# Performance work log

Measured on AMD Instinct MI355X. Metric: run time of the kernel, lower is better.

## Reference

```python
import jax, jax.numpy as jnp
import numpy as np

N = 50000      # nodes
E = 800000     # edges (before self-loops)
NFEAT = 128
NHID = 32
H = 8
NCLASS = 47
NEG_SLOPE = 0.2  # PyG GATv2Conv default


def gatv2_layer(x, src, dst, Wl, Wr, att, b, n):
    """One GATv2Conv layer (concat over heads). att: [H, C]."""
    h, c = att.shape
    xl = (x @ Wl).reshape(n, h, c)  # source transform (lin_l)
    xr = (x @ Wr).reshape(n, h, c)  # target transform (lin_r)
    e = jax.nn.leaky_relu(xl[src] + xr[dst], NEG_SLOPE)   # [E, H, C]
    logits = jnp.einsum('ehc,hc->eh', e, att)             # [E, H]
    # segment softmax over incoming edges of each target node
    m = jax.ops.segment_max(logits, dst, num_segments=n)  # [N, H]
    alpha = jnp.exp(logits - m[dst])
    denom = jax.ops.segment_sum(alpha, dst, num_segments=n)
    alpha = alpha / (denom[dst] + 1e-16)
    msg = xl[src] * alpha[:, :, None]                     # [E, H, C]
    out = jax.ops.segment_sum(msg, dst, num_segments=n)   # [N, H, C]
    return out.reshape(n, h * c) + b


def setup_inputs():
    key = jax.random.key(0)
    ks = jax.random.split(key, 16)
    s = 0.1
    x = jax.random.normal(ks[0], (N, NFEAT), jnp.float32)
    edge_index = jax.random.randint(ks[1], (2, E), 0, N)
    HID = H * NHID  # 256
    params = dict(
        Wl0=jax.random.normal(ks[2], (NFEAT, HID), jnp.float32) * s,
        Wr0=jax.random.normal(ks[3], (NFEAT, HID), jnp.float32) * s,
        a0=jax.random.normal(ks[4], (H, NHID), jnp.float32) * s,
        b0=jnp.zeros((HID,), jnp.float32),
        Wl1=jax.random.normal(ks[5], (HID, HID), jnp.float32) * s,
        Wr1=jax.random.normal(ks[6], (HID, HID), jnp.float32) * s,
        a1=jax.random.normal(ks[7], (H, NHID), jnp.float32) * s,
        b1=jnp.zeros((HID,), jnp.float32),
        Wl2=jax.random.normal(ks[8], (HID, NCLASS), jnp.float32) * s,
        Wr2=jax.random.normal(ks[9], (HID, NCLASS), jnp.float32) * s,
        a2=jax.random.normal(ks[10], (1, NCLASS), jnp.float32) * s,
        b2=jnp.zeros((NCLASS,), jnp.float32),
    )
    return {"x": x, "edge_index": edge_index, **params}


def reference(x, edge_index, Wl0, Wr0, a0, b0, Wl1, Wr1, a1, b1, Wl2, Wr2, a2, b2):
    n = x.shape[0]
    # PyG GATv2Conv adds self-loops by default
    loops = jnp.arange(n, dtype=edge_index.dtype)
    src = jnp.concatenate([edge_index[0], loops])
    dst = jnp.concatenate([edge_index[1], loops])
    h = gatv2_layer(x, src, dst, Wl0, Wr0, a0, b0, n)
    h = jax.nn.elu(h)
    h = gatv2_layer(h, src, dst, Wl1, Wr1, a1, b1, n)
    h = jax.nn.elu(h)
    h = gatv2_layer(h, src, dst, Wl2, Wr2, a2, b2, n)
    return jax.nn.log_softmax(h, axis=-1)
```

## Files before the change

kernel.cpp:

```cpp
#include <hip/hip_runtime.h>
#include <cmath>


#define NFEAT 128
#define HID 256
#define NCLS 47
#define L2PAD 64

typedef __attribute__((ext_vector_type(8))) short bf16x8;
typedef __attribute__((ext_vector_type(4))) float f32x4;
typedef __attribute__((ext_vector_type(2))) float f32x2;

__device__ __forceinline__ unsigned short f2b(float f) {
  unsigned int u = __builtin_bit_cast(unsigned int, f);
  u += 0x7FFFu + ((u >> 16) & 1u);
  return (unsigned short)(u >> 16);
}
__device__ __forceinline__ float b2f(unsigned short s) {
  return __builtin_bit_cast(float, (unsigned int)s << 16);
}
__device__ __forceinline__ f32x2 b2f2(unsigned int u) {
  return (f32x2){__builtin_bit_cast(float, u << 16),
                 __builtin_bit_cast(float, u & 0xFFFF0000u)};
}

__global__ void k_cast_bf16(const float* __restrict__ in,
                            unsigned short* __restrict__ out, int n4) {
  int i = blockIdx.x * blockDim.x + threadIdx.x;
  if (i < n4) {
    float4 v = reinterpret_cast<const float4*>(in)[i];
    ushort4 o = {f2b(v.x), f2b(v.y), f2b(v.z), f2b(v.w)};
    reinterpret_cast<ushort4*>(out)[i] = o;
  }
}

__global__ void k_wt(const float* __restrict__ W, unsigned short* __restrict__ WT,
                     int K, int M, int Mpad) {
  int i = blockIdx.x * blockDim.x + threadIdx.x;
  if (i >= Mpad * K) return;
  int m = i / K, k = i - m * K;
  WT[i] = (m < M) ? f2b(W[(size_t)k * M + m]) : 0;
}

__global__ void k_pad_att(const float* __restrict__ a, float* __restrict__ out48) {
  int i = threadIdx.x;
  if (i < 48) out48[i] = (i < NCLS) ? a[i] : 0.f;
}

__global__ void k_init_deg(int* __restrict__ deg, int n) {
  int i = blockIdx.x * blockDim.x + threadIdx.x;
  if (i < n) deg[i] = 1;
}

__global__ void k_count(const int* __restrict__ dst, int* __restrict__ deg, int e) {
  int i = blockIdx.x * blockDim.x + threadIdx.x;
  if (i < e) atomicAdd(&deg[dst[i]], 1);
}

__global__ __launch_bounds__(256) void k_bsum(const int* __restrict__ deg,
                                              int* __restrict__ bsum, int n) {
  int t = threadIdx.x;
  int base = blockIdx.x * 1024 + t * 4;
  int s = 0;
  if (base + 3 < n) {
    int4 v = *reinterpret_cast<const int4*>(deg + base);
    s = v.x + v.y + v.z + v.w;
  } else {
    for (int j = 0; j < 4; ++j) { int i = base + j; if (i < n) s += deg[i]; }
  }
  #pragma unroll
  for (int off = 1; off < 64; off <<= 1) s += __shfl_xor(s, off, 64);
  __shared__ int wsum[4];
  if ((t & 63) == 0) wsum[t >> 6] = s;
  __syncthreads();
  if (t == 0) bsum[blockIdx.x] = wsum[0] + wsum[1] + wsum[2] + wsum[3];
}

__global__ void k_scanb(int* __restrict__ bsum, int nb) {
  int lane = threadIdx.x;
  int v = (lane < nb) ? bsum[lane] : 0;
  #pragma unroll
  for (int off = 1; off < 64; off <<= 1) {
    int u = __shfl_up(v, off, 64);
    if (lane >= off) v += u;
  }
  if (lane < nb) bsum[lane] = v;
}

__global__ __launch_bounds__(256) void k_scanfinal(const int* __restrict__ deg,
                                                   const int* __restrict__ bscan,
                                                   int* __restrict__ rowptr, int n) {
  int t = threadIdx.x, b = blockIdx.x;
  int base = b * 1024 + t * 4;
  int v0 = 0, v1 = 0, v2 = 0, v3 = 0;
  if (base + 3 < n) {
    int4 v = *reinterpret_cast<const int4*>(deg + base);
    v0 = v.x; v1 = v.y; v2 = v.z; v3 = v.w;
  } else {
    if (base < n) v0 = deg[base];
    if (base + 1 < n) v1 = deg[base + 1];
    if (base + 2 < n) v2 = deg[base + 2];
    if (base + 3 < n) v3 = deg[base + 3];
  }
  int s = v0 + v1 + v2 + v3;
  int incl = s;
  #pragma unroll
  for (int off = 1; off < 64; off <<= 1) {
    int u = __shfl_up(incl, off, 64);
    if ((t & 63) >= off) incl += u;
  }
  __shared__ int wsum[4];
  int w = t >> 6, l = t & 63;
  if (l == 63) wsum[w] = incl;
  __syncthreads();
  int woff = 0;
  for (int j = 0; j < w; ++j) woff += wsum[j];
  int excl = incl - s + woff;
  int boff = (b == 0) ? 0 : bscan[b - 1];
  int p = boff + excl;
  if (base < n)     rowptr[base + 1] = p + v0;
  if (base + 1 < n) rowptr[base + 2] = p + v0 + v1;
  if (base + 2 < n) rowptr[base + 3] = p + v0 + v1 + v2;
  if (base + 3 < n) rowptr[base + 4] = p + v0 + v1 + v2 + v3;
  if (b == 0 && t == 0) rowptr[0] = 0;
}

__global__ void k_init_csr(const int* __restrict__ rowptr, int* __restrict__ adj,
                           int* __restrict__ vdst, int* __restrict__ cursor, int n) {
  int i = blockIdx.x * blockDim.x + threadIdx.x;
  if (i < n) { int p = rowptr[i]; adj[p] = i; vdst[p] = i; cursor[i] = p + 1; }
}

__global__ void k_scatter(const int* __restrict__ src, const int* __restrict__ dst,
                          int* __restrict__ cursor, int* __restrict__ adj,
                          int* __restrict__ vdst, int e) {
  int i = blockIdx.x * blockDim.x + threadIdx.x;
  if (i < e) {
    int d = dst[i];
    int p = atomicAdd(&cursor[d], 1);
    adj[p] = src[i];
    vdst[p] = d;
  }
}

__global__ __launch_bounds__(256) void gemm_dual_bf16(
    const unsigned short* __restrict__ X, const unsigned short* __restrict__ WlT,
    const unsigned short* __restrict__ WrT, unsigned short* __restrict__ XL,
    unsigned short* __restrict__ XR, int N, int K, int Mpad) {
  __shared__ __align__(16) unsigned short Xs[64][72];
  __shared__ __align__(16) unsigned short Ls[64][72];
  __shared__ __align__(16) unsigned short Rs[64][72];

  const int t = threadIdx.x;
  const int row0 = blockIdx.x * 64;
  const int col0 = blockIdx.y * 64;
  const int w = t >> 6, lane = t & 63;
  const int r15 = lane & 15, kc = lane >> 4;

  f32x4 accL[4], accR[4];
  #pragma unroll
  for (int i = 0; i < 4; ++i) {
    accL[i] = (f32x4){0.f, 0.f, 0.f, 0.f};
    accR[i] = (f32x4){0.f, 0.f, 0.f, 0.f};
  }

  for (int k0 = 0; k0 < K; k0 += 64) {
    #pragma unroll
    for (int cc = 0; cc < 2; ++cc) {
      int c = t + cc * 256;
      int row = c >> 3, seg = (c & 7) * 8;
      int grow = row0 + row;
      if (grow < N) {
        *reinterpret_cast<uint4*>(&Xs[row][seg]) =
            *reinterpret_cast<const uint4*>(X + (size_t)grow * K + k0 + seg);
      } else {
        *reinterpret_cast<uint4*>(&Xs[row][seg]) = (uint4){0, 0, 0, 0};
      }
      *reinterpret_cast<uint4*>(&Ls[row][seg]) =
          *reinterpret_cast<const uint4*>(WlT + (size_t)(col0 + row) * K + k0 + seg);
      *reinterpret_cast<uint4*>(&Rs[row][seg]) =
          *reinterpret_cast<const uint4*>(WrT + (size_t)(col0 + row) * K + k0 + seg);
    }
    __syncthreads();

    #pragma unroll
    for (int ks = 0; ks < 2; ++ks) {
      const bf16x8 a = *reinterpret_cast<const bf16x8*>(&Xs[16 * w + r15][ks * 32 + kc * 8]);
      #pragma unroll
      for (int nf = 0; nf < 4; ++nf) {
        const bf16x8 bl = *reinterpret_cast<const bf16x8*>(&Ls[nf * 16 + r15][ks * 32 + kc * 8]);
        const bf16x8 br = *reinterpret_cast<const bf16x8*>(&Rs[nf * 16 + r15][ks * 32 + kc * 8]);
        accL[nf] = __builtin_amdgcn_mfma_f32_16x16x32_bf16(a, bl, accL[nf], 0, 0, 0);
        accR[nf] = __builtin_amdgcn_mfma_f32_16x16x32_bf16(a, br, accR[nf], 0, 0, 0);
      }
    }
    __syncthreads();
  }

  #pragma unroll
  for (int nf = 0; nf < 4; ++nf) {
    int cc = col0 + nf * 16 + r15;
    #pragma unroll
    for (int i = 0; i < 4; ++i) {
      int rr = row0 + 16 * w + kc * 4 + i;
      if (rr < N) {
        XL[(size_t)rr * Mpad + cc] = f2b(accL[nf][i]);
        XR[(size_t)rr * Mpad + cc] = f2b(accR[nf][i]);
      }
    }
  }
}

__global__ __launch_bounds__(256) void gat_node_hc(
    const unsigned short* __restrict__ xl, const unsigned short* __restrict__ xr,
    const float* __restrict__ att, const float* __restrict__ bias,
    const int* __restrict__ rowptr, const int* __restrict__ adj,
    unsigned short* __restrict__ out, int n) {
  int wid = (blockIdx.x * blockDim.x + threadIdx.x) >> 6;
  int lane = threadIdx.x & 63;
  if (wid >= n) return;
  const int q = lane & 31, half = lane >> 5;

  const uint4 xrp = *reinterpret_cast<const uint4*>(xr + (size_t)wid * HID + q * 8);
  const f32x2 xr2[4] = {b2f2(xrp.x), b2f2(xrp.y), b2f2(xrp.z), b2f2(xrp.w)};
  const float4 af0 = *reinterpret_cast<const float4*>(att + q * 8);
  const float4 af1 = *reinterpret_cast<const float4*>(att + q * 8 + 4);
  const f32x2 a2[4] = {{af0.x, af0.y}, {af0.z, af0.w},
                       {af1.x, af1.y}, {af1.z, af1.w}};

  float m = -1e30f, denom = 0.f;
  f32x2 acc[4] = {{0.f, 0.f}, {0.f, 0.f}, {0.f, 0.f}, {0.f, 0.f}};

  const int beg = rowptr[wid], end = rowptr[wid + 1];
  for (int base = beg; base < end; base += 2) {
    const int i = base + half;
    const bool act = i < end;
    const int u = adj[act ? i : base];
    const uint4 p = *reinterpret_cast<const uint4*>(xl + (size_t)u * HID + q * 8);
    const f32x2 x2[4] = {b2f2(p.x), b2f2(p.y), b2f2(p.z), b2f2(p.w)};
    f32x2 s2 = x2[0] * 0.f;
    #pragma unroll
    for (int j = 0; j < 4; ++j) {
      f32x2 z = x2[j] + xr2[j];
      f32x2 lz = 0.2f * z;
      f32x2 r = {fmaxf(z.x, lz.x), fmaxf(z.y, lz.y)};
      s2 += r * a2[j];
    }
    float part = s2.x + s2.y;
    part += __shfl_xor(part, 1, 64);
    part += __shfl_xor(part, 2, 64);
    if (!act) part = -1e30f;
    if (__any(part > m + 8.f)) {
      float mn = fmaxf(m, part);
      float so = __expf(m - mn);
      float wn = act ? __expf(part - mn) : 0.f;
      denom = denom * so + wn;
      #pragma unroll
      for (int j = 0; j < 4; ++j) acc[j] = acc[j] * so + wn * x2[j];
      m = mn;
    } else {
      float wn = act ? __expf(part - m) : 0.f;
      denom += wn;
      #pragma unroll
      for (int j = 0; j < 4; ++j) acc[j] += wn * x2[j];
    }
  }

  float mo = __shfl_xor(m, 32, 64);
  float ms = fmaxf(m, mo);
  float sc = __expf(m - ms);
  denom *= sc;
  denom += __shfl_xor(denom, 32, 64);
  #pragma unroll
  for (int j = 0; j < 4; ++j) {
    acc[j] *= sc;
    acc[j].x += __shfl_xor(acc[j].x, 32, 64);
    acc[j].y += __shfl_xor(acc[j].y, 32, 64);
  }

  if (half == 0) {
    const float inv = 1.f / (denom + 1e-16f);
    const float4 bf0 = *reinterpret_cast<const float4*>(bias + q * 8);
    const float4 bf1 = *reinterpret_cast<const float4*>(bias + q * 8 + 4);
    float o[8] = {acc[0].x * inv + bf0.x, acc[0].y * inv + bf0.y,
                  acc[1].x * inv + bf0.z, acc[1].y * inv + bf0.w,
                  acc[2].x * inv + bf1.x, acc[2].y * inv + bf1.y,
                  acc[3].x * inv + bf1.z, acc[3].y * inv + bf1.w};
    #pragma unroll
    for (int j = 0; j < 8; ++j) o[j] = o[j] > 0.f ? o[j] : (__expf(o[j]) - 1.f);
    uint4 ov;
    ov.x = (unsigned)f2b(o[0]) | ((unsigned)f2b(o[1]) << 16);
    ov.y = (unsigned)f2b(o[2]) | ((unsigned)f2b(o[3]) << 16);
    ov.z = (unsigned)f2b(o[4]) | ((unsigned)f2b(o[5]) << 16);
    ov.w = (unsigned)f2b(o[6]) | ((unsigned)f2b(o[7]) << 16);
    *reinterpret_cast<uint4*>(out + (size_t)wid * HID + q * 8) = ov;
  }
}

__global__ __launch_bounds__(256) void k_logit_l2(
    const unsigned short* __restrict__ xl, const unsigned short* __restrict__ xr,
    const float* __restrict__ att48, const int* __restrict__ adj,
    const int* __restrict__ vdst, float* __restrict__ logit, int total) {
  int i = blockIdx.x * blockDim.x + threadIdx.x;
  if (i >= total) return;
  const int u = adj[i], v = vdst[i];
  const uint4* pu = reinterpret_cast<const uint4*>(xl + (size_t)u * L2PAD);
  const uint4* pv = reinterpret_cast<const uint4*>(xr + (size_t)v * L2PAD);
  f32x2 s2 = {0.f, 0.f};
  #pragma unroll
  for (int b = 0; b < 6; ++b) {
    const uint4 xu = pu[b], xv = pv[b];
    const f32x2* a2 = reinterpret_cast<const f32x2*>(att48 + b * 8);
    const unsigned ua[4] = {xu.x, xu.y, xu.z, xu.w};
    const unsigned va[4] = {xv.x, xv.y, xv.z, xv.w};
    #pragma unroll
    for (int j = 0; j < 4; ++j) {
      f32x2 z = b2f2(ua[j]) + b2f2(va[j]);
      f32x2 lz = 0.2f * z;
      f32x2 r = {fmaxf(z.x, lz.x), fmaxf(z.y, lz.y)};
      s2 += r * a2[j];
    }
  }
  logit[i] = s2.x + s2.y;
}

__global__ __launch_bounds__(256) void gat_node_l2(
    const unsigned short* __restrict__ xl, const float* __restrict__ logit,
    const float* __restrict__ bias, const int* __restrict__ rowptr,
    const int* __restrict__ adj, float* __restrict__ out, int n) {
  int wid = (blockIdx.x * blockDim.x + threadIdx.x) >> 6;
  int lane = threadIdx.x & 63;
  if (wid >= n) return;
  const bool act = lane < NCLS;
  const int beg = rowptr[wid], end = rowptr[wid + 1];

  float mx = -1e30f;
  for (int i = beg + lane; i < end; i += 64) mx = fmaxf(mx, logit[i]);
  #pragma unroll
  for (int off = 1; off < 64; off <<= 1) mx = fmaxf(mx, __shfl_xor(mx, off, 64));

  float denom = 0.f, acc = 0.f;
  int i = beg;
  for (; i + 1 < end; i += 2) {
    int u0 = adj[i], u1 = adj[i + 1];
    float w0 = __expf(logit[i] - mx);
    float w1 = __expf(logit[i + 1] - mx);
    float x0 = act ? b2f(xl[(size_t)u0 * L2PAD + lane]) : 0.f;
    float x1 = act ? b2f(xl[(size_t)u1 * L2PAD + lane]) : 0.f;
    denom += w0 + w1;
    acc += w0 * x0 + w1 * x1;
  }
  if (i < end) {
    int u0 = adj[i];
    float w0 = __expf(logit[i] - mx);
    float x0 = act ? b2f(xl[(size_t)u0 * L2PAD + lane]) : 0.f;
    denom += w0;
    acc += w0 * x0;
  }

  float r = acc / (denom + 1e-16f) + (act ? bias[lane] : 0.f);
  float rm = act ? r : -1e30f;
  #pragma unroll
  for (int off = 1; off < 64; off <<= 1) rm = fmaxf(rm, __shfl_xor(rm, off, 64));
  float se = act ? __expf(r - rm) : 0.f;
  #pragma unroll
  for (int off = 1; off < 64; off <<= 1) se += __shfl_xor(se, off, 64);
  if (act) out[(size_t)wid * NCLS + lane] = r - rm - __logf(se);
}

extern "C" void kernel_launch(void* const* d_in, const int* in_sizes, int n_in,
                              void* d_out, int out_size, void* d_ws, size_t ws_size,
                              hipStream_t stream) {
  const float* x   = (const float*)d_in[0];
  const int* ei    = (const int*)d_in[1];
  const float* Wl0 = (const float*)d_in[2];
  const float* Wr0 = (const float*)d_in[3];
  const float* a0  = (const float*)d_in[4];
  const float* b0  = (const float*)d_in[5];
  const float* Wl1 = (const float*)d_in[6];
  const float* Wr1 = (const float*)d_in[7];
  const float* a1  = (const float*)d_in[8];
  const float* b1  = (const float*)d_in[9];
  const float* Wl2 = (const float*)d_in[10];
  const float* Wr2 = (const float*)d_in[11];
  const float* a2  = (const float*)d_in[12];
  const float* b2  = (const float*)d_in[13];

  const int N = in_sizes[0] / NFEAT;
  const int E = in_sizes[1] / 2;
  const int* src = ei;
  const int* dst = ei + E;
  const int total = E + N;

  char* ws = (char*)d_ws;
  unsigned short* xlb = (unsigned short*)ws; ws += (size_t)N * HID * 2;
  unsigned short* xrb = (unsigned short*)ws; ws += (size_t)N * HID * 2;
  unsigned short* xb  = (unsigned short*)ws; ws += (size_t)N * HID * 2;
  unsigned short* hb  = (unsigned short*)ws; ws += (size_t)N * HID * 2;
  unsigned short* WT  = (unsigned short*)ws; ws += (size_t)6 * HID * HID * 2;
  float* logit = (float*)ws; ws += (size_t)total * sizeof(float);
  float* att48 = (float*)ws; ws += 64 * sizeof(float);
  int* deg    = (int*)ws; ws += (size_t)N * sizeof(int);
  int* rowptr = (int*)ws; ws += (size_t)(N + 8) * sizeof(int);
  int* bsum   = (int*)ws; ws += (size_t)64 * sizeof(int);
  int* adj    = (int*)ws; ws += (size_t)total * sizeof(int);
  int* vdst   = (int*)ws; ws += (size_t)total * sizeof(int);

  unsigned short* WlT0 = WT + 0 * HID * HID;
  unsigned short* WrT0 = WT + 1 * HID * HID;
  unsigned short* WlT1 = WT + 2 * HID * HID;
  unsigned short* WrT1 = WT + 3 * HID * HID;
  unsigned short* WlT2 = WT + 4 * HID * HID;
  unsigned short* WrT2 = WT + 5 * HID * HID;

  const int TB = 256;
  const int nbScan = (N + 1023) / 1024;

  k_cast_bf16<<<(N * NFEAT / 4 + TB - 1) / TB, TB, 0, stream>>>(x, xb, N * NFEAT / 4);
  k_wt<<<(HID * NFEAT + TB - 1) / TB, TB, 0, stream>>>(Wl0, WlT0, NFEAT, HID, HID);
  k_wt<<<(HID * NFEAT + TB - 1) / TB, TB, 0, stream>>>(Wr0, WrT0, NFEAT, HID, HID);
  k_wt<<<(HID * HID + TB - 1) / TB, TB, 0, stream>>>(Wl1, WlT1, HID, HID, HID);
  k_wt<<<(HID * HID + TB - 1) / TB, TB, 0, stream>>>(Wr1, WrT1, HID, HID, HID);
  k_wt<<<(L2PAD * HID + TB - 1) / TB, TB, 0, stream>>>(Wl2, WlT2, HID, NCLS, L2PAD);
  k_wt<<<(L2PAD * HID + TB - 1) / TB, TB, 0, stream>>>(Wr2, WrT2, HID, NCLS, L2PAD);
  k_pad_att<<<1, 64, 0, stream>>>(a2, att48);

  k_init_deg<<<(N + TB - 1) / TB, TB, 0, stream>>>(deg, N);
  k_count<<<(E + TB - 1) / TB, TB, 0, stream>>>(dst, deg, E);
  k_bsum<<<nbScan, TB, 0, stream>>>(deg, bsum, N);
  k_scanb<<<1, 64, 0, stream>>>(bsum, nbScan);
  k_scanfinal<<<nbScan, TB, 0, stream>>>(deg, bsum, rowptr, N);
  k_init_csr<<<(N + TB - 1) / TB, TB, 0, stream>>>(rowptr, adj, vdst, deg, N);
  k_scatter<<<(E + TB - 1) / TB, TB, 0, stream>>>(src, dst, deg, adj, vdst, E);

  const int nodeBlocks = (N + 3) / 4;
  const int rowBlocks = (N + 63) / 64;

  {
    dim3 g(rowBlocks, HID / 64);
    gemm_dual_bf16<<<g, 256, 0, stream>>>(xb, WlT0, WrT0, xlb, xrb, N, NFEAT, HID);
    gat_node_hc<<<nodeBlocks, 256, 0, stream>>>(xlb, xrb, a0, b0, rowptr, adj, hb, N);
  }
  {
    dim3 g(rowBlocks, HID / 64);
    gemm_dual_bf16<<<g, 256, 0, stream>>>(hb, WlT1, WrT1, xlb, xrb, N, HID, HID);
    gat_node_hc<<<nodeBlocks, 256, 0, stream>>>(xlb, xrb, a1, b1, rowptr, adj, xb, N);
  }
  {
    dim3 g(rowBlocks, 1);
    gemm_dual_bf16<<<g, 256, 0, stream>>>(xb, WlT2, WrT2, xlb, xrb, N, HID, L2PAD);
    k_logit_l2<<<(total + TB - 1) / TB, TB, 0, stream>>>(xlb, xrb, att48, adj,
                                                         vdst, logit, total);
    gat_node_l2<<<nodeBlocks, 256, 0, stream>>>(xlb, logit, b2, rowptr, adj,
                                                (float*)d_out, N);
  }
}
```

Measured before the change: 445.1 us.

## Use direct global-to-LDS loads with XOR swizzle, unroll edge loop, merge weight transposes

```diff
diff --git a/kernel.cpp b/kernel.cpp
--- a/kernel.cpp
+++ b/kernel.cpp
@@ -24,6 +24,12 @@
                  __builtin_bit_cast(float, u & 0xFFFF0000u)};
 }
 
+__device__ __forceinline__ void glds16(const unsigned short* g, unsigned short* l) {
+  __builtin_amdgcn_global_load_lds(
+      (const __attribute__((address_space(1))) unsigned int*)g,
+      (__attribute__((address_space(3))) unsigned int*)l, 16, 0, 0);
+}
+
 __global__ void k_cast_bf16(const float* __restrict__ in,
                             unsigned short* __restrict__ out, int n4) {
   int i = blockIdx.x * blockDim.x + threadIdx.x;
@@ -34,12 +40,21 @@
   }
 }
 
-__global__ void k_wt(const float* __restrict__ W, unsigned short* __restrict__ WT,
-                     int K, int M, int Mpad) {
-  int i = blockIdx.x * blockDim.x + threadIdx.x;
-  if (i >= Mpad * K) return;
-  int m = i / K, k = i - m * K;
-  WT[i] = (m < M) ? f2b(W[(size_t)k * M + m]) : 0;
+struct WtArgs {
+  const float* W[6];
+  unsigned short* WT[6];
+  int K[6], M[6], off[6], total;
+};
+__global__ void k_wt_all(WtArgs a) {
+  int i = blockIdx.x * blockDim.x + threadIdx.x;
+  if (i >= a.total) return;
+  int s = 0;
+  #pragma unroll
+  for (int j = 1; j < 6; ++j) if (i >= a.off[j]) s = j;
+  int jj = i - a.off[s];
+  int K = a.K[s], M = a.M[s];
+  int m = jj / K, k = jj - m * K;
+  a.WT[s][jj] = (m < M) ? f2b(a.W[s][(size_t)k * M + m]) : (unsigned short)0;
 }
 
 __global__ void k_pad_att(const float* __restrict__ a, float* __restrict__ out48) {
@@ -147,15 +162,24 @@
     const unsigned short* __restrict__ X, const unsigned short* __restrict__ WlT,
     const unsigned short* __restrict__ WrT, unsigned short* __restrict__ XL,
     unsigned short* __restrict__ XR, int N, int K, int Mpad) {
-  __shared__ __align__(16) unsigned short Xs[64][72];
-  __shared__ __align__(16) unsigned short Ls[64][72];
-  __shared__ __align__(16) unsigned short Rs[64][72];
+  __shared__ __align__(16) unsigned short S[3 * 64 * 64];
+  unsigned short* Xs = S;
+  unsigned short* Ls = S + 4096;
+  unsigned short* Rs = S + 8192;
 
   const int t = threadIdx.x;
-  const int row0 = blockIdx.x * 64;
-  const int col0 = blockIdx.y * 64;
+  const int col0 = blockIdx.x * 64;
+  const int row0 = blockIdx.y * 64;
   const int w = t >> 6, lane = t & 63;
   const int r15 = lane & 15, kc = lane >> 4;
+  const bool tail = (row0 + 64 > N);
+
+  const int rowa = t >> 3, c16a = t & 7;
+  const int rowb = (t + 256) >> 3, c16b = t & 7;
+  const int sga = (c16a ^ (rowa & 7)) * 8;
+  const int sgb = (c16b ^ (rowb & 7)) * 8;
+  unsigned short* ldst0 = S + (w * 512);
+  unsigned short* ldst1 = S + (2048 + w * 512);
 
   f32x4 accL[4], accR[4];
   #pragma unroll
@@ -164,32 +188,38 @@
     accR[i] = (f32x4){0.f, 0.f, 0.f, 0.f};
   }
 
+  const int rA = 16 * w + r15;
+
   for (int k0 = 0; k0 < K; k0 += 64) {
-    #pragma unroll
-    for (int cc = 0; cc < 2; ++cc) {
-      int c = t + cc * 256;
-      int row = c >> 3, seg = (c & 7) * 8;
-      int grow = row0 + row;
-      if (grow < N) {
-        *reinterpret_cast<uint4*>(&Xs[row][seg]) =
-            *reinterpret_cast<const uint4*>(X + (size_t)grow * K + k0 + seg);
-      } else {
-        *reinterpret_cast<uint4*>(&Xs[row][seg]) = (uint4){0, 0, 0, 0};
-      }
-      *reinterpret_cast<uint4*>(&Ls[row][seg]) =
-          *reinterpret_cast<const uint4*>(WlT + (size_t)(col0 + row) * K + k0 + seg);
-      *reinterpret_cast<uint4*>(&Rs[row][seg]) =
-          *reinterpret_cast<const uint4*>(WrT + (size_t)(col0 + row) * K + k0 + seg);
+    glds16(WlT + (size_t)(col0 + rowa) * K + k0 + sga, ldst0 + 4096);
+    glds16(WlT + (size_t)(col0 + rowb) * K + k0 + sgb, ldst1 + 4096);
+    glds16(WrT + (size_t)(col0 + rowa) * K + k0 + sga, ldst0 + 8192);
+    glds16(WrT + (size_t)(col0 + rowb) * K + k0 + sgb, ldst1 + 8192);
+    if (!tail) {
+      glds16(X + (size_t)(row0 + rowa) * K + k0 + sga, ldst0);
+      glds16(X + (size_t)(row0 + rowb) * K + k0 + sgb, ldst1);
+    } else {
+      uint4 va = (uint4){0, 0, 0, 0}, vb = (uint4){0, 0, 0, 0};
+      if (row0 + rowa < N)
+        va = *reinterpret_cast<const uint4*>(X + (size_t)(row0 + rowa) * K + k0 + sga);
+      if (row0 + rowb < N)
+        vb = *reinterpret_cast<const uint4*>(X + (size_t)(row0 + rowb) * K + k0 + sgb);
+      *reinterpret_cast<uint4*>(Xs + rowa * 64 + c16a * 8) = va;
+      *reinterpret_cast<uint4*>(Xs + rowb * 64 + c16b * 8) = vb;
     }
     __syncthreads();
 
     #pragma unroll
     for (int ks = 0; ks < 2; ++ks) {
-      const bf16x8 a = *reinterpret_cast<const bf16x8*>(&Xs[16 * w + r15][ks * 32 + kc * 8]);
+      const int c16 = ks * 4 + kc;
+      const bf16x8 a = *reinterpret_cast<const bf16x8*>(
+          Xs + rA * 64 + ((c16 ^ (rA & 7)) * 8));
       #pragma unroll
       for (int nf = 0; nf < 4; ++nf) {
-        const bf16x8 bl = *reinterpret_cast<const bf16x8*>(&Ls[nf * 16 + r15][ks * 32 + kc * 8]);
-        const bf16x8 br = *reinterpret_cast<const bf16x8*>(&Rs[nf * 16 + r15][ks * 32 + kc * 8]);
+        const int rB = nf * 16 + r15;
+        const int so = rB * 64 + ((c16 ^ (rB & 7)) * 8);
+        const bf16x8 bl = *reinterpret_cast<const bf16x8*>(Ls + so);
+        const bf16x8 br = *reinterpret_cast<const bf16x8*>(Rs + so);
         accL[nf] = __builtin_amdgcn_mfma_f32_16x16x32_bf16(a, bl, accL[nf], 0, 0, 0);
         accR[nf] = __builtin_amdgcn_mfma_f32_16x16x32_bf16(a, br, accR[nf], 0, 0, 0);
       }
@@ -232,37 +262,69 @@
   f32x2 acc[4] = {{0.f, 0.f}, {0.f, 0.f}, {0.f, 0.f}, {0.f, 0.f}};
 
   const int beg = rowptr[wid], end = rowptr[wid + 1];
-  for (int base = beg; base < end; base += 2) {
-    const int i = base + half;
-    const bool act = i < end;
-    const int u = adj[act ? i : base];
-    const uint4 p = *reinterpret_cast<const uint4*>(xl + (size_t)u * HID + q * 8);
-    const f32x2 x2[4] = {b2f2(p.x), b2f2(p.y), b2f2(p.z), b2f2(p.w)};
-    f32x2 s2 = x2[0] * 0.f;
-    #pragma unroll
-    for (int j = 0; j < 4; ++j) {
-      f32x2 z = x2[j] + xr2[j];
-      f32x2 lz = 0.2f * z;
-      f32x2 r = {fmaxf(z.x, lz.x), fmaxf(z.y, lz.y)};
-      s2 += r * a2[j];
-    }
-    float part = s2.x + s2.y;
-    part += __shfl_xor(part, 1, 64);
-    part += __shfl_xor(part, 2, 64);
-    if (!act) part = -1e30f;
-    if (__any(part > m + 8.f)) {
-      float mn = fmaxf(m, part);
-      float so = __expf(m - mn);
-      float wn = act ? __expf(part - mn) : 0.f;
-      denom = denom * so + wn;
+  for (int base = beg; base < end; base += 4) {
+    const int e0 = base + half, e1 = base + 2 + half;
+    const bool act0 = e0 < end, act1 = e1 < end;
+    const int u0 = adj[act0 ? e0 : beg];
+    const int u1 = adj[act1 ? e1 : beg];
+    const uint4 p0 = *reinterpret_cast<const uint4*>(xl + (size_t)u0 * HID + q * 8);
+    const uint4 p1 = *reinterpret_cast<const uint4*>(xl + (size_t)u1 * HID + q * 8);
+    const f32x2 x0[4] = {b2f2(p0.x), b2f2(p0.y), b2f2(p0.z), b2f2(p0.w)};
+    const f32x2 x1[4] = {b2f2(p1.x), b2f2(p1.y), b2f2(p1.z), b2f2(p1.w)};
+    float part0, part1;
+    {
+      f32x2 s2 = {0.f, 0.f};
       #pragma unroll
-      for (int j = 0; j < 4; ++j) acc[j] = acc[j] * so + wn * x2[j];
-      m = mn;
+      for (int j = 0; j < 4; ++j) {
+        f32x2 z = x0[j] + xr2[j];
+        f32x2 lz = 0.2f * z;
+        f32x2 r = {fmaxf(z.x, lz.x), fmaxf(z.y, lz.y)};
+        s2 += r * a2[j];
+      }
+      part0 = s2.x + s2.y;
+      part0 += __shfl_xor(part0, 1, 64);
+      part0 += __shfl_xor(part0, 2, 64);
+      if (!act0) part0 = -1e30f;
+    }
+    {
+      f32x2 s2 = {0.f, 0.f};
+      #pragma unroll
+      for (int j = 0; j < 4; ++j) {
+        f32x2 z = x1[j] + xr2[j];
+        f32x2 lz = 0.2f * z;
+        f32x2 r = {fmaxf(z.x, lz.x), fmaxf(z.y, lz.y)};
+        s2 += r * a2[j];
+      }
+      part1 = s2.x + s2.y;
+      part1 += __shfl_xor(part1, 1, 64);
+      part1 += __shfl_xor(part1, 2, 64);
+      if (!act1) part1 = -1e30f;
+    }
+    if (__any(fmaxf(part0, part1) > m + 8.f)) {
+      {
+        float mn = fmaxf(m, part0);
+        float so = __expf(m - mn);
+        float wn = act0 ? __expf(part0 - mn) : 0.f;
+        denom = denom * so + wn;
+        #pragma unroll
+        for (int j = 0; j < 4; ++j) acc[j] = acc[j] * so + wn * x0[j];
+        m = mn;
+      }
+      {
+        float mn = fmaxf(m, part1);
+        float so = __expf(m - mn);
+        float wn = act1 ? __expf(part1 - mn) : 0.f;
+        denom = denom * so + wn;
+        #pragma unroll
+        for (int j = 0; j < 4; ++j) acc[j] = acc[j] * so + wn * x1[j];
+        m = mn;
+      }
     } else {
-      float wn = act ? __expf(part - m) : 0.f;
-      denom += wn;
+      float w0 = act0 ? __expf(part0 - m) : 0.f;
+      float w1 = act1 ? __expf(part1 - m) : 0.f;
+      denom += w0 + w1;
       #pragma unroll
-      for (int j = 0; j < 4; ++j) acc[j] += wn * x2[j];
+      for (int j = 0; j < 4; ++j) acc[j] += w0 * x0[j] + w1 * x1[j];
     }
   }
 
@@ -417,12 +479,21 @@
   const int nbScan = (N + 1023) / 1024;
 
   k_cast_bf16<<<(N * NFEAT / 4 + TB - 1) / TB, TB, 0, stream>>>(x, xb, N * NFEAT / 4);
-  k_wt<<<(HID * NFEAT + TB - 1) / TB, TB, 0, stream>>>(Wl0, WlT0, NFEAT, HID, HID);
-  k_wt<<<(HID * NFEAT + TB - 1) / TB, TB, 0, stream>>>(Wr0, WrT0, NFEAT, HID, HID);
-  k_wt<<<(HID * HID + TB - 1) / TB, TB, 0, stream>>>(Wl1, WlT1, HID, HID, HID);
-  k_wt<<<(HID * HID + TB - 1) / TB, TB, 0, stream>>>(Wr1, WrT1, HID, HID, HID);
-  k_wt<<<(L2PAD * HID + TB - 1) / TB, TB, 0, stream>>>(Wl2, WlT2, HID, NCLS, L2PAD);
-  k_wt<<<(L2PAD * HID + TB - 1) / TB, TB, 0, stream>>>(Wr2, WrT2, HID, NCLS, L2PAD);
+  {
+    WtArgs a;
+    const float* Wsrc[6] = {Wl0, Wr0, Wl1, Wr1, Wl2, Wr2};
+    unsigned short* Wdst[6] = {WlT0, WrT0, WlT1, WrT1, WlT2, WrT2};
+    int Ks[6] = {NFEAT, NFEAT, HID, HID, HID, HID};
+    int Ms[6] = {HID, HID, HID, HID, NCLS, NCLS};
+    int Mp[6] = {HID, HID, HID, HID, L2PAD, L2PAD};
+    int off = 0;
+    for (int s = 0; s < 6; ++s) {
+      a.W[s] = Wsrc[s]; a.WT[s] = Wdst[s]; a.K[s] = Ks[s]; a.M[s] = Ms[s];
+      a.off[s] = off; off += Mp[s] * Ks[s];
+    }
+    a.total = off;
+    k_wt_all<<<(a.total + TB - 1) / TB, TB, 0, stream>>>(a);
+  }
   k_pad_att<<<1, 64, 0, stream>>>(a2, att48);
 
   k_init_deg<<<(N + TB - 1) / TB, TB, 0, stream>>>(deg, N);
@@ -437,17 +508,17 @@
   const int rowBlocks = (N + 63) / 64;
 
   {
-    dim3 g(rowBlocks, HID / 64);
+    dim3 g(HID / 64, rowBlocks);
     gemm_dual_bf16<<<g, 256, 0, stream>>>(xb, WlT0, WrT0, xlb, xrb, N, NFEAT, HID);
     gat_node_hc<<<nodeBlocks, 256, 0, stream>>>(xlb, xrb, a0, b0, rowptr, adj, hb, N);
   }
   {
-    dim3 g(rowBlocks, HID / 64);
+    dim3 g(HID / 64, rowBlocks);
     gemm_dual_bf16<<<g, 256, 0, stream>>>(hb, WlT1, WrT1, xlb, xrb, N, HID, HID);
     gat_node_hc<<<nodeBlocks, 256, 0, stream>>>(xlb, xrb, a1, b1, rowptr, adj, xb, N);
   }
   {
-    dim3 g(rowBlocks, 1);
+    dim3 g(1, rowBlocks);
     gemm_dual_bf16<<<g, 256, 0, stream>>>(xb, WlT2, WrT2, xlb, xrb, N, HID, L2PAD);
     k_logit_l2<<<(total + TB - 1) / TB, TB, 0, stream>>>(xlb, xrb, att48, adj,
                                                          vdst, logit, total);
```

After: 425.7 us. -4.4%, faster.
